# Kernel optimization log

Hardware: AMD Instinct MI355X
Metric: run time of the kernel (lower is better)

The kernel has to match this reference:

```python
import jax, jax.numpy as jnp
import numpy as np

B, QL, CTX, H = 1, 2048, 2048, 4096
NH, NKV, HD = 32, 8, 128


def rotate_half(x):
    x1, x2 = jnp.split(x, 2, axis=-1)
    return jnp.concatenate([-x2, x1], axis=-1)


def apply_rotary(x, cos, sin):
    # x: [B, h, S, HD]; cos/sin: [B, S, HD] -> broadcast over heads
    cos = cos[:, None, :, :]
    sin = sin[:, None, :, :]
    return x * cos + rotate_half(x) * sin


def setup_inputs() -> dict:
    key = jax.random.key(0)
    ks = jax.random.split(key, 8)
    s = 0.02
    return {
        "hidden_states": jax.random.normal(ks[0], (B, QL, H), jnp.float32),
        "target_hidden": jax.random.normal(ks[1], (B, CTX, H), jnp.float32),
        "cos": jax.random.uniform(ks[2], (B, CTX + QL, HD), jnp.float32),
        "sin": jax.random.uniform(ks[3], (B, CTX + QL, HD), jnp.float32),
        "Wq": jax.random.normal(ks[4], (NH * HD, H), jnp.float32) * s,
        "Wk": jax.random.normal(ks[5], (NKV * HD, H), jnp.float32) * s,
        "Wv": jax.random.normal(ks[6], (NKV * HD, H), jnp.float32) * s,
        "Wo": jax.random.normal(ks[7], (H, NH * HD), jnp.float32) * s,
    }


def reference(hidden_states, target_hidden, cos, sin, Wq, Wk, Wv, Wo):
    bsz, q_len, _ = hidden_states.shape
    ctx_len = target_hidden.shape[1]

    def proj(x, W, nh):  # [B,S,H] @ W.T -> [B,nh,S,HD]
        y = jnp.einsum("bsh,dh->bsd", x, W)
        return y.reshape(bsz, x.shape[1], nh, HD).transpose(0, 2, 1, 3)

    q = proj(hidden_states, Wq, NH)
    k_ctx = proj(target_hidden, Wk, NKV)
    v_ctx = proj(target_hidden, Wv, NKV)
    k_noise = proj(hidden_states, Wk, NKV)
    v_noise = proj(hidden_states, Wv, NKV)

    cos_n = cos[:, ctx_len:ctx_len + q_len]
    sin_n = sin[:, ctx_len:ctx_len + q_len]
    q = apply_rotary(q, cos_n, sin_n)
    k_noise = apply_rotary(k_noise, cos_n, sin_n)
    k_ctx = apply_rotary(k_ctx, cos[:, :ctx_len], sin[:, :ctx_len])

    k = jnp.concatenate([k_ctx, k_noise], axis=2)  # [B,NKV,CTX+QL,HD]
    v = jnp.concatenate([v_ctx, v_noise], axis=2)

    n_rep = NH // NKV
    k = jnp.repeat(k, n_rep, axis=1)  # repeat_interleave on head dim
    v = jnp.repeat(v, n_rep, axis=1)

    scale = 1.0 / jnp.sqrt(jnp.asarray(HD, q.dtype))
    scores = jnp.einsum("bhqd,bhkd->bhqk", q, k) * scale
    probs = jax.nn.softmax(scores, axis=-1)
    attn = jnp.einsum("bhqk,bhkd->bhqd", probs, v)
    attn = attn.transpose(0, 2, 1, 3).reshape(bsz, q_len, NH * HD)
    return jnp.einsum("bsd,hd->bsh", attn, Wo)
```

## Files before the change

### kernel.cpp

```cpp
#include <hip/hip_runtime.h>

typedef unsigned short u16;
typedef _Float16 f16;
typedef _Float16 f16x4 __attribute__((ext_vector_type(4)));
typedef _Float16 f16x8 __attribute__((ext_vector_type(8)));
typedef float f32x4 __attribute__((ext_vector_type(4)));

#define GLL16(gptr, lptr)                                                        \
  __builtin_amdgcn_global_load_lds(                                              \
      (const __attribute__((address_space(1))) void*)(gptr),                     \
      (__attribute__((address_space(3))) void*)(lptr), 16, 0, 0)

__global__ void cast_all_k(const float* __restrict__ h, const float* __restrict__ t,
                           const float* __restrict__ wq, const float* __restrict__ wk,
                           const float* __restrict__ wv, const float* __restrict__ wo,
                           f16* __restrict__ Xcat, f16* __restrict__ Wqb,
                           f16* __restrict__ Wkvb, f16* __restrict__ Wob) {
  long i = (long)blockIdx.x * 256 + threadIdx.x;
  const float* s; f16* d; long off;
  if (i < 2097152)        { s = h;  d = Xcat;            off = i; }
  else if (i < 4194304)   { s = t;  d = Xcat + 8388608;  off = i - 2097152; }
  else if (i < 8388608)   { s = wq; d = Wqb;             off = i - 4194304; }
  else if (i < 9437184)   { s = wk; d = Wkvb;            off = i - 8388608; }
  else if (i < 10485760)  { s = wv; d = Wkvb + 4194304;  off = i - 9437184; }
  else                    { s = wo; d = Wob;             off = i - 10485760; }
  float4 v = *(const float4*)(s + off * 4);
  f16x4 o;
  o.x = (f16)v.x; o.y = (f16)v.y; o.z = (f16)v.z; o.w = (f16)v.w;
  *(f16x4*)(d + off * 4) = o;
}

template <int MODE>
__global__ __launch_bounds__(512, 2) void gemm8k(
    const f16* __restrict__ Xcat, const f16* __restrict__ Wqb,
    const f16* __restrict__ Wkvb, const float* __restrict__ cosT,
    const float* __restrict__ sinT, f16* __restrict__ Qb, f16* __restrict__ Kb,
    f16* __restrict__ Vt, const f16* __restrict__ Ao,
    const f16* __restrict__ Wob, float* __restrict__ Cp, float qscale) {
  __shared__ __align__(16) f16 lds[65536];
  const int tid = threadIdx.x;
  const int w = tid >> 6, lane = tid & 63;
  const int quad = lane >> 4, l16 = lane & 15;
  const int wm = w >> 1, wn = w & 1;

  int b = (int)blockIdx.x;
  int l = ((b & 7) << 5) | (b >> 3);

  const f16 *A, *B;
  long tM, tN;
  int NT, kbeg;
  bool isQ = false, isV = false;
  float* Cz = nullptr;
  if (MODE == 0) {
    kbeg = 0; NT = 64;
    if (l < 128) {
      A = Xcat; B = Wqb; tM = (long)(l >> 4) * 256; tN = (long)(l & 15) * 256;
      isQ = true;
    } else {
      int l2 = l - 128;
      A = Xcat; B = Wkvb; tM = (long)(l2 >> 3) * 256; tN = (long)(l2 & 7) * 256;
      isV = (tN >= 1024);
    }
  } else {
    int z = l >> 7, r0 = l & 127;
    A = Ao; B = Wob; tM = (long)(r0 >> 4) * 256; tN = (long)(r0 & 15) * 256;
    kbeg = z * 2048; NT = 32; Cz = Cp + (long)z * 8388608;
  }

  const int sr8 = lane >> 3;
  const int cg = (lane & 7) ^ sr8;
  const f16* Ag = A + (tM + 16 * w + sr8) * 4096 + kbeg + cg * 8;
  const f16* Bg = B + (tN + 16 * w + sr8) * 4096 + kbeg + cg * 8;
  const int ldsw = w * 1024;

#define STAGE_A(hf, t, c)                                                      \
  do {                                                                         \
    const f16* g_ = Ag + (long)(t) * 64 + (long)(hf) * (128 * 4096);           \
    f16* d_ = &lds[(c) * 16384 + (hf) * 8192 + ldsw];                          \
    GLL16(g_, d_);                                                             \
    GLL16(g_ + 8 * 4096, d_ + 512);                                            \
  } while (0)
#define STAGE_B(hf, t, c)                                                      \
  do {                                                                         \
    const f16* g_ = Bg + (long)(t) * 64 + (long)(hf) * (128 * 4096);           \
    f16* d_ = &lds[32768 + (c) * 16384 + (hf) * 8192 + ldsw];                  \
    GLL16(g_, d_);                                                             \
    GLL16(g_ + 8 * 4096, d_ + 512);                                            \
  } while (0)

  const int rA = wm * 64 + l16;
  const int rB = wn * 128 + l16;
  const int sw = l16 & 7;
#define LDA(fr, mi, kk, c)                                                     \
  fr = *(const f16x8*)&lds[(c) * 16384 + (rA + (mi) * 16) * 64 +               \
                           (((kk) * 4 + quad) ^ sw) * 8]
#define LDB(fr, ni, kk, c)                                                     \
  fr = *(const f16x8*)&lds[32768 + (c) * 16384 + (rB + (ni) * 16) * 64 +       \
                           (((kk) * 4 + quad) ^ sw) * 8]

#define MFMA16 __builtin_amdgcn_mfma_f32_16x16x32_f16
#define BAR() __builtin_amdgcn_s_barrier()
#define WAITDS()                                                               \
  do {                                                                         \
    asm volatile("s_waitcnt lgkmcnt(0)" ::: "memory");                         \
    __builtin_amdgcn_sched_barrier(0);                                         \
  } while (0)

  f32x4 acc[4][8] = {};
  f16x8 af[2][2], bf0[4][2], bf1[4][2];

  STAGE_B(0, 0, 0); STAGE_B(1, 0, 0); STAGE_A(0, 0, 0); STAGE_A(1, 0, 0);
  STAGE_B(0, 1, 1); STAGE_B(1, 1, 1);
  asm volatile("s_waitcnt vmcnt(4)" ::: "memory");
  BAR();

#define TILE_STEP(t, c)                                                        \
  do {                                                                         \
                                       \
    LDA(af[0][0], 0, 0, c); LDA(af[0][1], 0, 1, c);                            \
    LDA(af[1][0], 1, 0, c); LDA(af[1][1], 1, 1, c);                            \
    LDB(bf0[0][0], 0, 0, c); LDB(bf0[0][1], 0, 1, c);                          \
    LDB(bf0[1][0], 1, 0, c); LDB(bf0[1][1], 1, 1, c);                          \
    LDB(bf0[2][0], 2, 0, c); LDB(bf0[2][1], 2, 1, c);                          \
    LDB(bf0[3][0], 3, 0, c); LDB(bf0[3][1], 3, 1, c);                          \
    if ((t) + 1 < NT) STAGE_A(0, (t) + 1, (c) ^ 1);                            \
    BAR(); WAITDS();                                                           \
    __builtin_amdgcn_s_setprio(1);                                             \
    _Pragma("unroll") for (int mi = 0; mi < 2; ++mi)                           \
        _Pragma("unroll") for (int ni = 0; ni < 4; ++ni) {                     \
      acc[mi][ni] = MFMA16(af[mi][0], bf0[ni][0], acc[mi][ni], 0, 0, 0);       \
      acc[mi][ni] = MFMA16(af[mi][1], bf0[ni][1], acc[mi][ni], 0, 0, 0);       \
    }                                                                          \
    __builtin_amdgcn_s_setprio(0);                                             \
    BAR();                                                                     \
                                       \
    LDB(bf1[0][0], 4, 0, c); LDB(bf1[0][1], 4, 1, c);                          \
    LDB(bf1[1][0], 5, 0, c); LDB(bf1[1][1], 5, 1, c);                          \
    LDB(bf1[2][0], 6, 0, c); LDB(bf1[2][1], 6, 1, c);                          \
    LDB(bf1[3][0], 7, 0, c); LDB(bf1[3][1], 7, 1, c);                          \
    if ((t) + 1 < NT) STAGE_A(1, (t) + 1, (c) ^ 1);                            \
    BAR(); WAITDS();                                                           \
    __builtin_amdgcn_s_setprio(1);                                             \
    _Pragma("unroll") for (int mi = 0; mi < 2; ++mi)                           \
        _Pragma("unroll") for (int ni = 0; ni < 4; ++ni) {                     \
      acc[mi][4 + ni] =                                                        \
          MFMA16(af[mi][0], bf1[ni][0], acc[mi][4 + ni], 0, 0, 0);             \
      acc[mi][4 + ni] =                                                        \
          MFMA16(af[mi][1], bf1[ni][1], acc[mi][4 + ni], 0, 0, 0);             \
    }                                                                          \
    __builtin_amdgcn_s_setprio(0);                                             \
    BAR();                                                                     \
                                       \
    LDA(af[0][0], 2, 0, c); LDA(af[0][1], 2, 1, c);                            \
    LDA(af[1][0], 3, 0, c); LDA(af[1][1], 3, 1, c);                            \
    if ((t) + 2 < NT) STAGE_B(0, (t) + 2, c);                                  \
    BAR(); WAITDS();                                                           \
    __builtin_amdgcn_s_setprio(1);                                             \
    _Pragma("unroll") for (int mi = 0; mi < 2; ++mi)                           \
        _Pragma("unroll") for (int ni = 0; ni < 4; ++ni) {                     \
      acc[2 + mi][ni] = MFMA16(af[mi][0], bf0[ni][0], acc[2 + mi][ni], 0, 0, 0);\
      acc[2 + mi][ni] = MFMA16(af[mi][1], bf0[ni][1], acc[2 + mi][ni], 0, 0, 0);\
    }                                                                          \
    __builtin_amdgcn_s_setprio(0);                                             \
    BAR();                                                                     \
      \
    if ((t) + 2 < NT) STAGE_B(1, (t) + 2, c);                                  \
    BAR();                                                                     \
    __builtin_amdgcn_s_setprio(1);                                             \
    _Pragma("unroll") for (int mi = 0; mi < 2; ++mi)                           \
        _Pragma("unroll") for (int ni = 0; ni < 4; ++ni) {                     \
      acc[2 + mi][4 + ni] =                                                    \
          MFMA16(af[mi][0], bf1[ni][0], acc[2 + mi][4 + ni], 0, 0, 0);         \
      acc[2 + mi][4 + ni] =                                                    \
          MFMA16(af[mi][1], bf1[ni][1], acc[2 + mi][4 + ni], 0, 0, 0);         \
    }                                                                          \
    __builtin_amdgcn_s_setprio(0);                                             \
    if ((t) + 2 < NT)                                                          \
      asm volatile("s_waitcnt vmcnt(4)" ::: "memory");                         \
    else                                                                       \
      asm volatile("s_waitcnt vmcnt(0)" ::: "memory");                         \
    BAR();                                                                     \
  } while (0)

  for (int t = 0; t < NT; t += 2) {
    TILE_STEP(t, 0);
    TILE_STEP(t + 1, 1);
  }

  if (MODE == 1) {
#pragma unroll
    for (int mi = 0; mi < 4; ++mi)
#pragma unroll
      for (int ni = 0; ni < 8; ++ni)
#pragma unroll
        for (int r = 0; r < 4; ++r) {
          long row = tM + wm * 64 + mi * 16 + quad * 4 + r;
          long col = tN + wn * 128 + ni * 16 + l16;
          Cz[row * 4096 + col] = acc[mi][ni][r];
        }
  } else if (isV) {
    const int kvh = (int)((tN - 1024) >> 7) + wn;
#pragma unroll
    for (int mi = 0; mi < 4; ++mi) {
      int key0 = ((int)tM + wm * 64 + mi * 16 + quad * 4) ^ 2048;
#pragma unroll
      for (int ni = 0; ni < 8; ++ni) {
        int d = ni * 16 + l16;
        f16x4 pk;
#pragma unroll
        for (int r = 0; r < 4; ++r) pk[r] = (f16)acc[mi][ni][r];
        *(f16x4*)&Vt[((long)kvh * 128 + d) * 4096 + key0] = pk;
      }
    }
  } else {
    const float sc = isQ ? qscale : 1.0f;
    const int h = (int)(tN >> 7) + wn;
#pragma unroll
    for (int mi = 0; mi < 4; ++mi)
#pragma unroll
      for (int r = 0; r < 4; ++r) {
        int rg = (int)tM + wm * 64 + mi * 16 + quad * 4 + r;
        int pos = isQ ? (2048 + rg) : (rg ^ 2048);
        const float* cp = cosT + (long)pos * 128;
        const float* sp = sinT + (long)pos * 128;
        f16* orow = isQ ? Qb + ((long)h * 2048 + rg) * 128
                        : Kb + ((long)h * 4096 + pos) * 128;
#pragma unroll
        for (int ni = 0; ni < 4; ++ni) {
          int d = ni * 16 + l16;
          float x0 = acc[mi][ni][r], x1 = acc[mi][ni + 4][r];
          orow[d] = (f16)((x0 * cp[d] - x1 * sp[d]) * sc);
          orow[d + 64] = (f16)((x1 * cp[d + 64] + x0 * sp[d + 64]) * sc);
        }
      }
  }
#undef TILE_STEP
#undef STAGE_A
#undef STAGE_B
#undef LDA
#undef LDB
#undef WAITDS
#undef BAR
#undef MFMA16
}

__global__ __launch_bounds__(256, 2) void flash_k(const f16* __restrict__ Qb,
                                                  const f16* __restrict__ Kb,
                                                  const f16* __restrict__ Vt,
                                                  f16* __restrict__ Ob) {
  __shared__ __align__(16) f16 Ks[2][64 * 128];
  __shared__ __align__(16) f16 Vs[128 * 64];
  __shared__ __align__(16) f16 Ps[4][32 * 72];
  const int tid = threadIdx.x;
  const int w = tid >> 6, lane = tid & 63;
  const int quad = lane >> 4, l16 = lane & 15;
  const int b = blockIdx.x;
  const int kvh = b & 7;
  const int j = b >> 3;
  const int h = kvh * 4 + (j >> 4);
  const int q0 = (j & 15) * 128;

  f16x8 qf[2][4];
#pragma unroll
  for (int mi = 0; mi < 2; ++mi) {
    const f16* qrow = Qb + ((long)h * 2048 + q0 + w * 32 + mi * 16 + l16) * 128 + quad * 8;
#pragma unroll
    for (int kc = 0; kc < 4; ++kc) qf[mi][kc] = *(const f16x8*)(qrow + kc * 32);
  }

  f32x4 of[2][8] = {};
  float lsum[2] = {0.f, 0.f};
  const f16* Kg = Kb + (long)kvh * 4096 * 128;
  const f16* Vg = Vt + (long)kvh * 128 * 4096;
  f16* PsW = &Ps[w][0];

  const int krow = (lane >> 4);
  const int kslot = lane & 15;
  const int vrow = (lane >> 3);
  const int vslot = lane & 7;
  const int vgc = vslot ^ (vrow & 7);

#define FBAR() __builtin_amdgcn_s_barrier()
#define STAGE_K(kt_, c_)                                                       \
  do {                                                                         \
    _Pragma("unroll") for (int it = 0; it < 4; ++it) {                         \
      int row = w * 16 + it * 4 + krow;                                        \
      int gc = kslot ^ (it * 4 + krow);                                        \
      GLL16(Kg + (long)((kt_)*64 + row) * 128 + gc * 8,                        \
            &Ks[c_][(w * 16 + it * 4) * 128]);                                 \
    }                                                                          \
  } while (0)
#define STAGE_V(kt_)                                                           \
  do {                                                                         \
    _Pragma("unroll") for (int it = 0; it < 4; ++it) {                         \
      int row = w * 32 + it * 8 + vrow;                                        \
      GLL16(Vg + (long)row * 4096 + (kt_)*64 + vgc * 8,                        \
            &Vs[(w * 32 + it * 8) * 64]);                                      \
    }                                                                          \
  } while (0)

#define QKT(dst, c_)                                                           \
  do {                                                                         \
    _Pragma("unroll") for (int nt = 0; nt < 4; ++nt) {                         \
      f16x8 ak[4];                                                             \
      _Pragma("unroll") for (int kc = 0; kc < 4; ++kc) {                       \
        int slot = (kc * 4 + quad) ^ l16;                                      \
        ak[kc] = *(const f16x8*)&Ks[c_][(nt * 16 + l16) * 128 + slot * 8];     \
      }                                                                        \
      _Pragma("unroll") for (int mi = 0; mi < 2; ++mi)                         \
          _Pragma("unroll") for (int kc = 0; kc < 4; ++kc)                     \
        dst[mi][nt] = __builtin_amdgcn_mfma_f32_16x16x32_f16(                  \
            ak[kc], qf[mi][kc], dst[mi][nt], 0, 0, 0);                         \
    }                                                                          \
  } while (0)

#define EXPP(src)                                                              \
  do {                                                                         \
    _Pragma("unroll") for (int mi = 0; mi < 2; ++mi)                           \
        _Pragma("unroll") for (int nt = 0; nt < 4; ++nt) {                     \
      f16x4 pk;                                                                \
      _Pragma("unroll") for (int r = 0; r < 4; ++r) {                          \
        float pv = __builtin_amdgcn_exp2f(src[mi][nt][r]);                     \
        lsum[mi] += pv;                                                        \
        pk[r] = (f16)pv;                                                       \
      }                                                                        \
      *(f16x4*)&PsW[(mi * 16 + l16) * 72 + nt * 16 + quad * 4] = pk;           \
    }                                                                          \
  } while (0)

#define PVACC()                                                                \
  do {                                                                         \
    _Pragma("unroll") for (int kc2 = 0; kc2 < 2; ++kc2) {                      \
      f16x8 bp[2];                                                             \
      _Pragma("unroll") for (int mi = 0; mi < 2; ++mi)                         \
        bp[mi] = *(const f16x8*)&PsW[(mi * 16 + l16) * 72 + kc2 * 32 +         \
                                     quad * 8];                                \
      _Pragma("unroll") for (int dt = 0; dt < 8; ++dt) {                       \
        int slot = (kc2 * 4 + quad) ^ (l16 & 7);                               \
        f16x8 av = *(const f16x8*)&Vs[(dt * 16 + l16) * 64 + slot * 8];        \
        _Pragma("unroll") for (int mi = 0; mi < 2; ++mi)                       \
          of[mi][dt] = __builtin_amdgcn_mfma_f32_16x16x32_f16(                 \
              av, bp[mi], of[mi][dt], 0, 0, 0);                                \
      }                                                                        \
    }                                                                          \
  } while (0)

  f32x4 sP[2][4] = {};
  f32x4 sC[2][4];

  STAGE_K(0, 0);
  asm volatile("s_waitcnt vmcnt(0)" ::: "memory");
  FBAR();
  __builtin_amdgcn_s_setprio(1);
  QKT(sP, 0);
  __builtin_amdgcn_s_setprio(0);
  STAGE_K(1, 1);
  STAGE_V(0);

  for (int kt = 1; kt < 64; ++kt) {
    const int c = kt & 1;
    asm volatile("s_waitcnt vmcnt(4)" ::: "memory");
    FBAR();

#pragma unroll
    for (int mi = 0; mi < 2; ++mi)
#pragma unroll
      for (int nt = 0; nt < 4; ++nt) sC[mi][nt] = f32x4{0.f, 0.f, 0.f, 0.f};
    __builtin_amdgcn_s_setprio(1);
    QKT(sC, c);
    EXPP(sP);
    __builtin_amdgcn_s_setprio(0);

    if (kt < 63) STAGE_K(kt + 1, c ^ 1);
    if (kt < 63)
      asm volatile("s_waitcnt vmcnt(4)" ::: "memory");
    else
      asm volatile("s_waitcnt vmcnt(0)" ::: "memory");
    FBAR();

    __builtin_amdgcn_s_setprio(1);
    PVACC();
    __builtin_amdgcn_s_setprio(0);

    FBAR();
    STAGE_V(kt);

#pragma unroll
    for (int mi = 0; mi < 2; ++mi)
#pragma unroll
      for (int nt = 0; nt < 4; ++nt) sP[mi][nt] = sC[mi][nt];
  }

  EXPP(sP);
  asm volatile("s_waitcnt vmcnt(0)" ::: "memory");
  FBAR();
  PVACC();

#undef STAGE_K
#undef STAGE_V
#undef QKT
#undef EXPP
#undef PVACC
#undef FBAR

#pragma unroll
  for (int mi = 0; mi < 2; ++mi) {
    float v = lsum[mi];
    v += __shfl_xor(v, 16, 64);
    v += __shfl_xor(v, 32, 64);
    float inv = 1.0f / v;
    long q = q0 + w * 32 + mi * 16 + l16;
#pragma unroll
    for (int dt = 0; dt < 8; ++dt) {
      f16x4 o4;
#pragma unroll
      for (int r = 0; r < 4; ++r) o4[r] = (f16)(of[mi][dt][r] * inv);
      *(f16x4*)&Ob[q * 4096 + h * 128 + dt * 16 + quad * 4] = o4;
    }
  }
}

__global__ void reduce2_k(const float* __restrict__ p, float* __restrict__ out) {
  long i = ((long)blockIdx.x * 256 + threadIdx.x) * 4;
  float4 a = *(const float4*)(p + i);
  float4 b = *(const float4*)(p + 8388608 + i);
  a.x += b.x; a.y += b.y; a.z += b.z; a.w += b.w;
  *(float4*)(out + i) = a;
}

extern "C" void kernel_launch(void* const* d_in, const int* in_sizes, int n_in,
                              void* d_out, int out_size, void* d_ws, size_t ws_size,
                              hipStream_t stream) {
  (void)in_sizes; (void)n_in; (void)out_size; (void)ws_size;
  const float* hidden = (const float*)d_in[0];
  const float* target = (const float*)d_in[1];
  const float* cosT = (const float*)d_in[2];
  const float* sinT = (const float*)d_in[3];
  const float* Wq = (const float*)d_in[4];
  const float* Wk = (const float*)d_in[5];
  const float* Wv = (const float*)d_in[6];
  const float* Wo = (const float*)d_in[7];
  float* out = (float*)d_out;

  char* p = (char*)d_ws;
  auto alloc = [&](size_t bytes) {
    char* r = p;
    p += (bytes + 255) & ~(size_t)255;
    return r;
  };
  f16* Xcat = (f16*)alloc(4096ull * 4096 * 2);
  f16* Wqb  = (f16*)alloc(4096ull * 4096 * 2);
  f16* Wkvb = (f16*)alloc(2048ull * 4096 * 2);
  f16* Wob  = (f16*)alloc(4096ull * 4096 * 2);
  f16* Qb   = (f16*)alloc(32ull * 2048 * 128 * 2);
  f16* Kb   = (f16*)alloc(8ull * 4096 * 128 * 2);
  f16* Vt   = (f16*)alloc(8ull * 128 * 4096 * 2);
  f16* Ao   = (f16*)alloc(2048ull * 4096 * 2);
  float* Pp = (float*)d_ws;

  cast_all_k<<<57344, 256, 0, stream>>>(hidden, target, Wq, Wk, Wv, Wo,
                                        Xcat, Wqb, Wkvb, Wob);

  const float QSC = (float)(0.08838834764831845 * 1.4426950408889634);
  gemm8k<0><<<256, 512, 0, stream>>>(Xcat, Wqb, Wkvb, cosT, sinT, Qb, Kb, Vt,
                                     nullptr, nullptr, nullptr, QSC);

  flash_k<<<512, 256, 0, stream>>>(Qb, Kb, Vt, Ao);

  gemm8k<1><<<256, 512, 0, stream>>>(nullptr, nullptr, nullptr, nullptr, nullptr,
                                     nullptr, nullptr, nullptr, Ao, Wob, Pp, 0.f);
  reduce2_k<<<8192, 256, 0, stream>>>(Pp, out);
}
```

Baseline: 583.1 us.

## Double-buffer V in flash attention and merge per-iteration barriers

Gives the V tile the same two shared-memory buffers as K and prefetches both K and V one tile ahead, so each iteration needs two barriers instead of four and fewer vmcnt waits. The loop is unrolled by two with ping-pong score registers, removing the sP=sC copy. The P scratch buffer loses its row padding and uses an XOR swizzle to avoid bank conflicts. In exchange, shared memory per block grows by 16 KB, which may limit occupancy at two blocks per CU.

```diff
diff --git a/kernel.cpp b/kernel.cpp
--- a/kernel.cpp
+++ b/kernel.cpp
@@ -249,8 +249,8 @@
                                                   const f16* __restrict__ Vt,
                                                   f16* __restrict__ Ob) {
   __shared__ __align__(16) f16 Ks[2][64 * 128];
-  __shared__ __align__(16) f16 Vs[128 * 64];
-  __shared__ __align__(16) f16 Ps[4][32 * 72];
+  __shared__ __align__(16) f16 Vs[2][128 * 64];
+  __shared__ __align__(16) f16 Ps[4][32 * 64];
   const int tid = threadIdx.x;
   const int w = tid >> 6, lane = tid & 63;
   const int quad = lane >> 4, l16 = lane & 15;
@@ -273,6 +273,7 @@
   const f16* Kg = Kb + (long)kvh * 4096 * 128;
   const f16* Vg = Vt + (long)kvh * 128 * 4096;
   f16* PsW = &Ps[w][0];
+  const int psw = l16 & 7;
 
   const int krow = (lane >> 4);
   const int kslot = lane & 15;
@@ -290,12 +291,12 @@
             &Ks[c_][(w * 16 + it * 4) * 128]);                                 \
     }                                                                          \
   } while (0)
-#define STAGE_V(kt_)                                                           \
+#define STAGE_V(kt_, c_)                                                       \
   do {                                                                         \
     _Pragma("unroll") for (int it = 0; it < 4; ++it) {                         \
       int row = w * 32 + it * 8 + vrow;                                        \
       GLL16(Vg + (long)row * 4096 + (kt_)*64 + vgc * 8,                        \
-            &Vs[(w * 32 + it * 8) * 64]);                                      \
+            &Vs[c_][(w * 32 + it * 8) * 64]);                                  \
     }                                                                          \
   } while (0)
 
@@ -324,20 +325,22 @@
         lsum[mi] += pv;                                                        \
         pk[r] = (f16)pv;                                                       \
       }                                                                        \
-      *(f16x4*)&PsW[(mi * 16 + l16) * 72 + nt * 16 + quad * 4] = pk;           \
-    }                                                                          \
-  } while (0)
-
-#define PVACC()                                                                \
+      *(f16x4*)&PsW[(mi * 16 + l16) * 64 +                                     \
+                    (((nt * 2 + (quad >> 1)) ^ psw) << 3) + ((quad & 1) << 2)] \
+          = pk;                                                                \
+    }                                                                          \
+  } while (0)
+
+#define PVACC(vb_)                                                             \
   do {                                                                         \
     _Pragma("unroll") for (int kc2 = 0; kc2 < 2; ++kc2) {                      \
       f16x8 bp[2];                                                             \
       _Pragma("unroll") for (int mi = 0; mi < 2; ++mi)                         \
-        bp[mi] = *(const f16x8*)&PsW[(mi * 16 + l16) * 72 + kc2 * 32 +         \
-                                     quad * 8];                                \
+        bp[mi] = *(const f16x8*)&PsW[(mi * 16 + l16) * 64 +                    \
+                                     (((kc2 * 4 + quad) ^ psw) << 3)];         \
       _Pragma("unroll") for (int dt = 0; dt < 8; ++dt) {                       \
         int slot = (kc2 * 4 + quad) ^ (l16 & 7);                               \
-        f16x8 av = *(const f16x8*)&Vs[(dt * 16 + l16) * 64 + slot * 8];        \
+        f16x8 av = *(const f16x8*)&Vs[vb_][(dt * 16 + l16) * 64 + slot * 8];   \
         _Pragma("unroll") for (int mi = 0; mi < 2; ++mi)                       \
           of[mi][dt] = __builtin_amdgcn_mfma_f32_16x16x32_f16(                 \
               av, bp[mi], of[mi][dt], 0, 0, 0);                                \
@@ -345,57 +348,56 @@
     }                                                                          \
   } while (0)
 
-  f32x4 sP[2][4] = {};
-  f32x4 sC[2][4];
-
-  STAGE_K(0, 0);
+#define ZEROS(s_)                                                              \
+  do {                                                                         \
+    _Pragma("unroll") for (int mi = 0; mi < 2; ++mi)                           \
+        _Pragma("unroll") for (int nt = 0; nt < 4; ++nt)                       \
+            s_[mi][nt] = f32x4{0.f, 0.f, 0.f, 0.f};                            \
+  } while (0)
+
+#define ITER(kt_, c_, sPrev, sCur)                                             \
+  do {                                                                         \
+    asm volatile("s_waitcnt vmcnt(4)" ::: "memory");         \
+    FBAR();                                                                    \
+    __builtin_amdgcn_sched_barrier(0);                                         \
+    ZEROS(sCur);                                                               \
+    __builtin_amdgcn_s_setprio(1);                                             \
+    QKT(sCur, c_);                                                             \
+    EXPP(sPrev);                                                               \
+    PVACC((c_) ^ 1);                                                           \
+    __builtin_amdgcn_s_setprio(0);                                             \
+    FBAR();                                                                    \
+    if ((kt_) < 63) {                                                          \
+      STAGE_K((kt_) + 1, (c_) ^ 1);                                            \
+      STAGE_V((kt_) + 1, (c_) ^ 1);                                            \
+    }                                                                          \
+  } while (0)
+
+  f32x4 sA[2][4], sB[2][4];
+
+  STAGE_K(0, 0); STAGE_V(0, 0);
+  STAGE_K(1, 1); STAGE_V(1, 1);
+  asm volatile("s_waitcnt vmcnt(8)" ::: "memory");
+  FBAR();
+  __builtin_amdgcn_sched_barrier(0);
+  ZEROS(sA);
+  __builtin_amdgcn_s_setprio(1);
+  QKT(sA, 0);
+  __builtin_amdgcn_s_setprio(0);
+
+  for (int kt = 1; kt < 63; kt += 2) {
+    ITER(kt, 1, sA, sB);
+    ITER(kt + 1, 0, sB, sA);
+  }
+  ITER(63, 1, sA, sB);
+
+  EXPP(sB);
   asm volatile("s_waitcnt vmcnt(0)" ::: "memory");
   FBAR();
-  __builtin_amdgcn_s_setprio(1);
-  QKT(sP, 0);
-  __builtin_amdgcn_s_setprio(0);
-  STAGE_K(1, 1);
-  STAGE_V(0);
-
-  for (int kt = 1; kt < 64; ++kt) {
-    const int c = kt & 1;
-    asm volatile("s_waitcnt vmcnt(4)" ::: "memory");
-    FBAR();
-
-#pragma unroll
-    for (int mi = 0; mi < 2; ++mi)
-#pragma unroll
-      for (int nt = 0; nt < 4; ++nt) sC[mi][nt] = f32x4{0.f, 0.f, 0.f, 0.f};
-    __builtin_amdgcn_s_setprio(1);
-    QKT(sC, c);
-    EXPP(sP);
-    __builtin_amdgcn_s_setprio(0);
-
-    if (kt < 63) STAGE_K(kt + 1, c ^ 1);
-    if (kt < 63)
-      asm volatile("s_waitcnt vmcnt(4)" ::: "memory");
-    else
-      asm volatile("s_waitcnt vmcnt(0)" ::: "memory");
-    FBAR();
-
-    __builtin_amdgcn_s_setprio(1);
-    PVACC();
-    __builtin_amdgcn_s_setprio(0);
-
-    FBAR();
-    STAGE_V(kt);
-
-#pragma unroll
-    for (int mi = 0; mi < 2; ++mi)
-#pragma unroll
-      for (int nt = 0; nt < 4; ++nt) sP[mi][nt] = sC[mi][nt];
-  }
-
-  EXPP(sP);
-  asm volatile("s_waitcnt vmcnt(0)" ::: "memory");
-  FBAR();
-  PVACC();
-
+  PVACC(1);
+
+#undef ITER
+#undef ZEROS
 #undef STAGE_K
 #undef STAGE_V
 #undef QKT
```

Measured after the change: 607.1 us. 4.1% more time.
